# Kernel optimization log

Hardware: AMD Instinct MI355X
Metric: run time of the kernel (lower is better)

The kernel has to match this reference:

```python
import jax, jax.numpy as jnp
import numpy as np

B, S, E = 2, 8192, 128


def setup_inputs() -> dict:
    key = jax.random.key(0)
    ks = jax.random.split(key, 7)
    sc = 1.0 / np.sqrt(E)
    return {
        "x": jax.random.normal(ks[0], (B, S, E), dtype=jnp.float32),
        "Wq": jax.random.normal(ks[1], (E, E), dtype=jnp.float32) * sc,
        "bq": jax.random.normal(ks[2], (E,), dtype=jnp.float32) * 0.01,
        "Wk": jax.random.normal(ks[3], (E, E), dtype=jnp.float32) * sc,
        "bk": jax.random.normal(ks[4], (E,), dtype=jnp.float32) * 0.01,
        "Wv": jax.random.normal(ks[5], (E, E), dtype=jnp.float32) * sc,
        "bv": jax.random.normal(ks[6], (E,), dtype=jnp.float32) * 0.01,
    }


def reference(x, Wq, bq, Wk, bk, Wv, bv):
    # x: [B, S, E]. Conv1d(k=1) == per-slice linear: out[b,s,o] = sum_e W[o,e] x[b,s,e] + b[o]
    embed_dim = x.shape[-1]
    Q = jnp.einsum("bse,oe->bso", x, Wq) + bq  # [B, S, E]
    K = jnp.einsum("bse,oe->bso", x, Wk) + bk
    V = jnp.einsum("bse,oe->bso", x, Wv) + bv
    scores = jnp.einsum("bsd,btd->bst", Q, K) / jnp.sqrt(
        jnp.asarray(embed_dim, dtype=x.dtype)
    )  # [B, S, S]
    A = jax.nn.softmax(scores, axis=-1)
    # torch: out = bmm(V^T_as[B,E,S], A^T)[.transpose] == sum_t A[b,s,t] V[b,t,e]
    out = jnp.einsum("bst,bte->bse", A, V)  # [B, S, E]
    return out
```

## Files before the change

### kernel.cpp

```cpp
#include <hip/hip_runtime.h>
#include <math.h>

#define NB 2
#define NS 8192
#define NE 128
#define NROWS (NB * NS)

typedef __attribute__((ext_vector_type(8))) short s8v;
typedef __attribute__((ext_vector_type(16))) float fx16;
typedef __attribute__((ext_vector_type(2))) unsigned int u2v;
typedef __attribute__((address_space(1))) const unsigned char as1c;
typedef __attribute__((address_space(3))) unsigned char as3t;

static __device__ __forceinline__ unsigned int pkbf(float a, float b) {
    unsigned int ua = __float_as_uint(a), ub = __float_as_uint(b);
    ua += 0x7FFFu + ((ua >> 16) & 1u);
    ub += 0x7FFFu + ((ub >> 16) & 1u);
    return (ua >> 16) | (ub & 0xFFFF0000u);
}

static __device__ __forceinline__ unsigned int cvtpk(float a, float b) {
    unsigned int r;
    asm("v_cvt_pk_bf16_f32 %0, %1, %2" : "=v"(r) : "v"(a), "v"(b));
    return r;
}

static __device__ __forceinline__ void split8(const float* p, uint4& H, uint4& L) {
    float4 a = *(const float4*)p;
    float4 b = *(const float4*)(p + 4);
    unsigned int h0 = cvtpk(a.x, a.y), h1 = cvtpk(a.z, a.w);
    unsigned int h2 = cvtpk(b.x, b.y), h3 = cvtpk(b.z, b.w);
    H = make_uint4(h0, h1, h2, h3);
    float l0 = a.x - __uint_as_float(h0 << 16);
    float l1 = a.y - __uint_as_float(h0 & 0xFFFF0000u);
    float l2 = a.z - __uint_as_float(h1 << 16);
    float l3 = a.w - __uint_as_float(h1 & 0xFFFF0000u);
    float l4 = b.x - __uint_as_float(h2 << 16);
    float l5 = b.y - __uint_as_float(h2 & 0xFFFF0000u);
    float l6 = b.z - __uint_as_float(h3 << 16);
    float l7 = b.w - __uint_as_float(h3 & 0xFFFF0000u);
    L = make_uint4(cvtpk(l0, l1), cvtpk(l2, l3), cvtpk(l4, l5), cvtpk(l6, l7));
}

__global__ __launch_bounds__(256, 4)
void split_kernel(const float* __restrict__ x,
                  const float* __restrict__ Wq, const float* __restrict__ Wk,
                  const float* __restrict__ Wv,
                  unsigned short* __restrict__ xh, unsigned short* __restrict__ xl,
                  unsigned short* __restrict__ WhS, unsigned short* __restrict__ WlS)
{
    const int bid = blockIdx.x;
    if (bid < 1024) {
        const int i = (bid * 256 + threadIdx.x) * 8;
        uint4 H, L;
        split8(&x[i], H, L);
        *(uint4*)&xh[i] = H;
        *(uint4*)&xl[i] = L;
    } else {
        const int tid = (bid - 1024) * 256 + threadIdx.x;
        const int mat = tid >> 11;
        const int rem = tid & 2047;
        const int r = rem >> 4, g = rem & 15;
        const float* W = (mat == 0) ? Wq : (mat == 1) ? Wk : Wv;
        uint4 H, L;
        split8(&W[r * 128 + g * 8], H, L);
        const int gs = g ^ (r & 7);
        *(uint4*)&WhS[mat * 16384 + r * 128 + gs * 8] = H;
        *(uint4*)&WlS[mat * 16384 + r * 128 + gs * 8] = L;
    }
}

__global__ __launch_bounds__(256, 2)
void qkv_kernel(const unsigned short* __restrict__ xh,
                const unsigned short* __restrict__ xl,
                const unsigned short* __restrict__ WhS,
                const unsigned short* __restrict__ WlS,
                const float* __restrict__ bq, const float* __restrict__ bk,
                const float* __restrict__ bv,
                unsigned short* __restrict__ qkv)
{
    __shared__ unsigned short xhL[64 * 128];
    __shared__ unsigned short xlL[64 * 128];
    __shared__ unsigned short WhL[64 * 128];
    __shared__ unsigned short WlL[64 * 128];

    const int t    = threadIdx.x;
    const int rblk = blockIdx.x * 64;
    const int mat  = blockIdx.y;
    const int o0   = blockIdx.z * 64;

    const float* bias = (mat == 0) ? bq : (mat == 1) ? bk : bv;
    unsigned short* out = qkv + (size_t)mat * NROWS * NE;
    const float osc = (mat == 0) ? 0.1275174460620886f : 1.0f;

    const int w = t >> 6, lane = t & 63, lq = lane & 31, h = lane >> 5;

    if (w < 2) {
        const unsigned short* src = (w == 0) ? xh : xl;
        unsigned short* dst = (w == 0) ? xhL : xlL;
        const int rb4 = lane >> 4;
        const int cg  = lane & 15;
        #pragma unroll
        for (int i = 0; i < 16; ++i) {
            const int row = 4 * i + rb4;
            const int c   = cg ^ (row & 7);
            __builtin_amdgcn_global_load_lds(
                (as1c*)(src + (size_t)(rblk + row) * NE + c * 8),
                (as3t*)(dst + i * 512 + lane * 8), 16, 0, 0);
        }
    } else {
        const unsigned short* src = ((w == 2) ? WhS : WlS) + mat * 16384 + o0 * 128;
        unsigned short* dst = (w == 2) ? WhL : WlL;
        #pragma unroll
        for (int i = 0; i < 16; ++i) {
            __builtin_amdgcn_global_load_lds(
                (as1c*)(src + i * 512 + lane * 8),
                (as3t*)(dst + i * 512 + lane * 8), 16, 0, 0);
        }
    }
    __syncthreads();

    const int rloc = (w & 1) * 32;
    const int ot   = w >> 1;

    s8v xhf[8], xlf[8], whf[8], wlf[8];
    #pragma unroll
    for (int s = 0; s < 8; ++s) {
        const int cx = ((s * 2 + h) ^ (lq & 7)) * 8;
        xhf[s] = *(const s8v*)&xhL[(rloc + lq) * 128 + cx];
        xlf[s] = *(const s8v*)&xlL[(rloc + lq) * 128 + cx];
        whf[s] = *(const s8v*)&WhL[(ot * 32 + lq) * 128 + cx];
        wlf[s] = *(const s8v*)&WlL[(ot * 32 + lq) * 128 + cx];
    }

    fx16 acc;
    #pragma unroll
    for (int i = 0; i < 16; ++i) acc[i] = 0.f;

    #pragma unroll
    for (int s = 0; s < 8; ++s) {
        if (mat != 2) {
            acc = __builtin_amdgcn_mfma_f32_32x32x16_bf16(whf[s], xhf[s], acc, 0, 0, 0);
            acc = __builtin_amdgcn_mfma_f32_32x32x16_bf16(whf[s], xlf[s], acc, 0, 0, 0);
            acc = __builtin_amdgcn_mfma_f32_32x32x16_bf16(wlf[s], xhf[s], acc, 0, 0, 0);
        } else {
            acc = __builtin_amdgcn_mfma_f32_32x32x16_bf16(xhf[s], whf[s], acc, 0, 0, 0);
            acc = __builtin_amdgcn_mfma_f32_32x32x16_bf16(xlf[s], whf[s], acc, 0, 0, 0);
            acc = __builtin_amdgcn_mfma_f32_32x32x16_bf16(xhf[s], wlf[s], acc, 0, 0, 0);
        }
    }

    __syncthreads();
    unsigned short* TB = xhL;

    if (mat != 2) {
        #pragma unroll
        for (int g = 0; g < 4; ++g) {
            const int ob = o0 + ot * 32 + 4 * h + 8 * g;
            float4 bb = *(const float4*)&bias[ob];
            float v0 = (acc[4 * g + 0] + bb.x) * osc;
            float v1 = (acc[4 * g + 1] + bb.y) * osc;
            float v2 = (acc[4 * g + 2] + bb.z) * osc;
            float v3 = (acc[4 * g + 3] + bb.w) * osc;
            *(uint2*)&TB[(rloc + lq) * 72 + ot * 32 + 4 * h + 8 * g] =
                make_uint2(pkbf(v0, v1), pkbf(v2, v3));
        }
        __syncthreads();
        #pragma unroll
        for (int it = 0; it < 2; ++it) {
            const int r2 = it * 32 + (t >> 3);
            const int c2 = (t & 7) * 8;
            uint4 vv = *(const uint4*)&TB[r2 * 72 + c2];
            *(uint4*)&out[(size_t)(rblk + r2) * NE + o0 + c2] = vv;
        }
    } else {
        const float bv_ = bias[o0 + ot * 32 + lq];
        #pragma unroll
        for (int g = 0; g < 4; ++g) {
            float v0 = acc[4 * g + 0] + bv_;
            float v1 = acc[4 * g + 1] + bv_;
            float v2 = acc[4 * g + 2] + bv_;
            float v3 = acc[4 * g + 3] + bv_;
            *(uint2*)&TB[(ot * 32 + lq) * 72 + rloc + 4 * h + 8 * g] =
                make_uint2(pkbf(v0, v1), pkbf(v2, v3));
        }
        __syncthreads();
        const int bb_ = rblk >> 13;
        #pragma unroll
        for (int it = 0; it < 2; ++it) {
            const int d2 = it * 32 + (t >> 3);
            const int kc = (t & 7) * 8;
            uint4 vv = *(const uint4*)&TB[d2 * 72 + kc];
            *(uint4*)&out[(((size_t)(bb_ * NE + o0 + d2)) << 13)
                          + (rblk & (NS - 1)) + kc] = vv;
        }
    }
}

__global__ __launch_bounds__(256, 2)
void attn_kernel(const unsigned short* __restrict__ qkv,
                 _Float16* __restrict__ pd,
                 _Float16* __restrict__ pw,
                 float* __restrict__ ml)
{
    __shared__ unsigned short kbuf[2][64 * 128];
    __shared__ unsigned short vbuf[2][64 * 128];

    const int t  = threadIdx.x;
    const int id = blockIdx.x;
    const int ks = id & 3;
    const int b  = (id >> 2) & 1;
    const int T  = id >> 3;

    const unsigned short* Qg = qkv;
    const unsigned short* Kg = qkv + (size_t)NROWS * NE;
    const unsigned short* Vb = qkv + (size_t)2 * NROWS * NE + ((size_t)b << 20);

    const int w = t >> 6, lane = t & 63, lq = lane & 31, h = lane >> 5;
    const int qbw = b * NS + T * 128 + w * 32;
    const size_t kvb = (size_t)b * NS * NE;
    const int kq0 = ks * 2048;

    s8v qf[8];
    #pragma unroll
    for (int s = 0; s < 8; ++s)
        qf[s] = *(const s8v*)(Qg + (size_t)(qbw + lq) * NE + s * 16 + h * 8);

    fx16 acc[4];
    #pragma unroll
    for (int dt = 0; dt < 4; ++dt)
        #pragma unroll
        for (int i = 0; i < 16; ++i) acc[dt][i] = 0.f;

    float l = 0.f;

    const unsigned short* gptr[8];
    if (w < 2) {
        #pragma unroll
        for (int j = 0; j < 8; ++j) {
            int i = 8 * w + j;
            int keyl = 4 * i + (lane >> 4);
            int c = (lane & 15) ^ (keyl & 7);
            gptr[j] = Kg + kvb + (size_t)(kq0 + keyl) * NE + c * 8;
        }
    } else {
        #pragma unroll
        for (int j = 0; j < 8; ++j) {
            int i = 8 * (w - 2) + j;
            int d = 8 * i + (lane >> 3);
            int g = (lane & 7) ^ (d & 7);
            gptr[j] = Vb + ((size_t)d << 13) + kq0 + g * 8;
        }
    }
    const int gstride = (w < 2) ? 64 * NE : 64;

    auto stage = [&](int bufi) {
        if (w < 2) {
            #pragma unroll
            for (int j = 0; j < 8; ++j) {
                __builtin_amdgcn_global_load_lds((as1c*)gptr[j],
                    (as3t*)&kbuf[bufi][(8 * w + j) * 512], 16, 0, 0);
                gptr[j] += gstride;
            }
        } else {
            #pragma unroll
            for (int j = 0; j < 8; ++j) {
                __builtin_amdgcn_global_load_lds((as1c*)gptr[j],
                    (as3t*)&vbuf[bufi][(8 * (w - 2) + j) * 512], 16, 0, 0);
                gptr[j] += gstride;
            }
        }
    };

    stage(0);
    __syncthreads();

#define PEX(i) (st2[(i) >> 4][(i) & 15])
    int buf = 0;
    const int swz = (lq & 7) * 8;

    for (int r = 0; r < 32; ++r) {
        if (r < 31) stage(buf ^ 1);

        fx16 st2[2];
        #pragma unroll
        for (int mt = 0; mt < 2; ++mt)
            #pragma unroll
            for (int i = 0; i < 16; ++i) st2[mt][i] = 0.f;
        __builtin_amdgcn_s_setprio(1);
        #pragma unroll
        for (int s = 0; s < 8; ++s) {
            int co = ((s * 2 + h) * 8) ^ swz;
            s8v a0 = *(const s8v*)&kbuf[buf][lq * 128 + co];
            s8v a1 = *(const s8v*)&kbuf[buf][(32 + lq) * 128 + co];
            st2[0] = __builtin_amdgcn_mfma_f32_32x32x16_bf16(a0, qf[s], st2[0], 0, 0, 0);
            st2[1] = __builtin_amdgcn_mfma_f32_32x32x16_bf16(a1, qf[s], st2[1], 0, 0, 0);
        }
        __builtin_amdgcn_s_setprio(0);

        float a0s = 0.f, a1s = 0.f, a2s = 0.f, a3s = 0.f;
        #pragma unroll
        for (int i = 0; i < 32; i += 4) {
            PEX(i)     = __builtin_amdgcn_exp2f(PEX(i));
            PEX(i + 1) = __builtin_amdgcn_exp2f(PEX(i + 1));
            PEX(i + 2) = __builtin_amdgcn_exp2f(PEX(i + 2));
            PEX(i + 3) = __builtin_amdgcn_exp2f(PEX(i + 3));
            a0s += PEX(i); a1s += PEX(i + 1); a2s += PEX(i + 2); a3s += PEX(i + 3);
        }
        float lsum = (a0s + a1s) + (a2s + a3s);
        lsum += __shfl_xor(lsum, 32);
        l += lsum;

        #pragma unroll
        for (int s2 = 0; s2 < 4; ++s2) {
            unsigned int P0 = cvtpk(PEX(s2 * 8 + 0), PEX(s2 * 8 + 1));
            unsigned int P1 = cvtpk(PEX(s2 * 8 + 2), PEX(s2 * 8 + 3));
            unsigned int P2 = cvtpk(PEX(s2 * 8 + 4), PEX(s2 * 8 + 5));
            unsigned int P3 = cvtpk(PEX(s2 * 8 + 6), PEX(s2 * 8 + 7));
            u2v r02 = __builtin_amdgcn_permlane32_swap(P0, P2, false, false);
            u2v r13 = __builtin_amdgcn_permlane32_swap(P1, P3, false, false);
            union { unsigned int u[4]; s8v v; } pf;
            pf.u[0] = r02.x;
            pf.u[1] = r13.x;
            pf.u[2] = r02.y;
            pf.u[3] = r13.y;
            int go = ((s2 * 2 + h) * 8) ^ swz;
            __builtin_amdgcn_s_setprio(1);
            #pragma unroll
            for (int dt = 0; dt < 4; ++dt) {
                s8v vf = *(const s8v*)&vbuf[buf][(lq + 32 * dt) * 64 + go];
                acc[dt] = __builtin_amdgcn_mfma_f32_32x32x16_bf16(pf.v, vf, acc[dt], 0, 0, 0);
            }
            __builtin_amdgcn_s_setprio(0);
        }

        __syncthreads();
        buf ^= 1;
    }
#undef PEX

    if (lane < 32)
        ml[(size_t)(qbw + lq) * 4 + ks] = l;

    float invl = 1.0f / l;
    _Float16* P = (ks < 2) ? pd : pw;
    const int slot = (ks & 1) * 128;
    #pragma unroll
    for (int rg = 0; rg < 16; ++rg) {
        int row = (rg & 3) + 8 * (rg >> 2) + 4 * h;
        float sc = __shfl(invl, row);
        size_t rb = (size_t)(qbw + row) * 256 + slot;
        #pragma unroll
        for (int dt = 0; dt < 4; ++dt)
            P[rb + lq + 32 * dt] = (_Float16)(acc[dt][rg] * sc);
    }
}

__global__ __launch_bounds__(256, 2)
void merge_kernel(const _Float16* __restrict__ pw,
                  const float* __restrict__ ml,
                  float* __restrict__ outp)
{
    const int gi = blockIdx.x * 256 + threadIdx.x;
    const int q = gi >> 4, d0 = (gi & 15) * 8;
    const _Float16* pd = (const _Float16*)outp;

    uint4 u0 = *(const uint4*)&pd[(size_t)q * 256 + d0];
    uint4 u1 = *(const uint4*)&pd[(size_t)q * 256 + 128 + d0];
    uint4 u2 = *(const uint4*)&pw[(size_t)q * 256 + d0];
    uint4 u3 = *(const uint4*)&pw[(size_t)q * 256 + 128 + d0];
    float l0 = ml[q * 4 + 0], l1 = ml[q * 4 + 1];
    float l2 = ml[q * 4 + 2], l3 = ml[q * 4 + 3];

    float inv = 1.f / (l0 + l1 + l2 + l3);
    float a0 = l0 * inv, a1 = l1 * inv, a2 = l2 * inv, a3 = l3 * inv;

    union { uint4 u; _Float16 hh[8]; } c0, c1, c2, c3;
    c0.u = u0; c1.u = u1; c2.u = u2; c3.u = u3;
    float ov[8];
    #pragma unroll
    for (int e = 0; e < 8; ++e)
        ov[e] = (float)c0.hh[e] * a0 + (float)c1.hh[e] * a1 +
                (float)c2.hh[e] * a2 + (float)c3.hh[e] * a3;

    *(float4*)&outp[(size_t)q * 128 + d0]     = *(float4*)&ov[0];
    *(float4*)&outp[(size_t)q * 128 + d0 + 4] = *(float4*)&ov[4];
}

extern "C" void kernel_launch(void* const* d_in, const int* in_sizes, int n_in,
                              void* d_out, int out_size, void* d_ws, size_t ws_size,
                              hipStream_t stream)
{
    const float* x  = (const float*)d_in[0];
    const float* Wq = (const float*)d_in[1];
    const float* bq = (const float*)d_in[2];
    const float* Wk = (const float*)d_in[3];
    const float* bk = (const float*)d_in[4];
    const float* Wv = (const float*)d_in[5];
    const float* bv = (const float*)d_in[6];
    float* out = (float*)d_out;

    unsigned char* ws = (unsigned char*)d_ws;
    unsigned short* qkv = (unsigned short*)ws;
    _Float16* pw = (_Float16*)(ws + (size_t)3 * NROWS * NE * 2);
    float* mlp = (float*)(ws + (size_t)3 * NROWS * NE * 2
                             + (size_t)NROWS * 256 * 2);
    unsigned char* ws2 = ws + (size_t)3 * NROWS * NE * 2
                            + (size_t)NROWS * 256 * 2 + (size_t)NROWS * 16;
    unsigned short* xh  = (unsigned short*)ws2;
    unsigned short* xl  = xh + (size_t)NROWS * NE;
    unsigned short* WhS = xl + (size_t)NROWS * NE;
    unsigned short* WlS = WhS + 3 * NE * NE;

    split_kernel<<<1048, 256, 0, stream>>>(x, Wq, Wk, Wv, xh, xl, WhS, WlS);

    dim3 g1(NROWS / 64, 3, 2);
    qkv_kernel<<<g1, 256, 0, stream>>>(xh, xl, WhS, WlS, bq, bk, bv, qkv);

    attn_kernel<<<512, 256, 0, stream>>>(qkv, (_Float16*)d_out, pw, mlp);
    merge_kernel<<<1024, 256, 0, stream>>>(pw, mlp, out);
}
```

Baseline: 164.1 us.

## Software-pipeline attention loop so next QK^T overlaps softmax and PV

Splits the per-tile loop into separate QK^T, softmax and PV stages and unrolls it by two with two score register sets. The QK^T MFMAs for the next key tile are issued while the current tile's exp and PV work proceeds. K and V staging are decoupled so K can be prefetched one tile ahead of V. The aim is to hide exp/transcendental latency and LDS waits behind matrix-core work, at the cost of extra registers, which may reduce occupancy.

```diff
diff --git a/kernel.cpp b/kernel.cpp
--- a/kernel.cpp
+++ b/kernel.cpp
@@ -254,7 +254,7 @@
     }
     const int gstride = (w < 2) ? 64 * NE : 64;
 
-    auto stage = [&](int bufi) {
+    auto stageK = [&](int bufi) {
         if (w < 2) {
             #pragma unroll
             for (int j = 0; j < 8; ++j) {
@@ -262,7 +262,10 @@
                     (as3t*)&kbuf[bufi][(8 * w + j) * 512], 16, 0, 0);
                 gptr[j] += gstride;
             }
-        } else {
+        }
+    };
+    auto stageV = [&](int bufi) {
+        if (w >= 2) {
             #pragma unroll
             for (int j = 0; j < 8; ++j) {
                 __builtin_amdgcn_global_load_lds((as1c*)gptr[j],
@@ -272,51 +275,49 @@
         }
     };
 
-    stage(0);
-    __syncthreads();
-
-#define PEX(i) (st2[(i) >> 4][(i) & 15])
-    int buf = 0;
     const int swz = (lq & 7) * 8;
 
-    for (int r = 0; r < 32; ++r) {
-        if (r < 31) stage(buf ^ 1);
-
-        fx16 st2[2];
+    auto gemm1 = [&](fx16 (&st)[2], int bufi) {
         #pragma unroll
         for (int mt = 0; mt < 2; ++mt)
             #pragma unroll
-            for (int i = 0; i < 16; ++i) st2[mt][i] = 0.f;
+            for (int i = 0; i < 16; ++i) st[mt][i] = 0.f;
         __builtin_amdgcn_s_setprio(1);
         #pragma unroll
         for (int s = 0; s < 8; ++s) {
             int co = ((s * 2 + h) * 8) ^ swz;
-            s8v a0 = *(const s8v*)&kbuf[buf][lq * 128 + co];
-            s8v a1 = *(const s8v*)&kbuf[buf][(32 + lq) * 128 + co];
-            st2[0] = __builtin_amdgcn_mfma_f32_32x32x16_bf16(a0, qf[s], st2[0], 0, 0, 0);
-            st2[1] = __builtin_amdgcn_mfma_f32_32x32x16_bf16(a1, qf[s], st2[1], 0, 0, 0);
+            s8v a0 = *(const s8v*)&kbuf[bufi][lq * 128 + co];
+            s8v a1 = *(const s8v*)&kbuf[bufi][(32 + lq) * 128 + co];
+            st[0] = __builtin_amdgcn_mfma_f32_32x32x16_bf16(a0, qf[s], st[0], 0, 0, 0);
+            st[1] = __builtin_amdgcn_mfma_f32_32x32x16_bf16(a1, qf[s], st[1], 0, 0, 0);
         }
         __builtin_amdgcn_s_setprio(0);
-
+    };
+
+#define PEX(st, i) (st[(i) >> 4][(i) & 15])
+    auto smax = [&](fx16 (&st)[2]) {
         float a0s = 0.f, a1s = 0.f, a2s = 0.f, a3s = 0.f;
         #pragma unroll
         for (int i = 0; i < 32; i += 4) {
-            PEX(i)     = __builtin_amdgcn_exp2f(PEX(i));
-            PEX(i + 1) = __builtin_amdgcn_exp2f(PEX(i + 1));
-            PEX(i + 2) = __builtin_amdgcn_exp2f(PEX(i + 2));
-            PEX(i + 3) = __builtin_amdgcn_exp2f(PEX(i + 3));
-            a0s += PEX(i); a1s += PEX(i + 1); a2s += PEX(i + 2); a3s += PEX(i + 3);
+            PEX(st, i)     = __builtin_amdgcn_exp2f(PEX(st, i));
+            PEX(st, i + 1) = __builtin_amdgcn_exp2f(PEX(st, i + 1));
+            PEX(st, i + 2) = __builtin_amdgcn_exp2f(PEX(st, i + 2));
+            PEX(st, i + 3) = __builtin_amdgcn_exp2f(PEX(st, i + 3));
+            a0s += PEX(st, i); a1s += PEX(st, i + 1);
+            a2s += PEX(st, i + 2); a3s += PEX(st, i + 3);
         }
         float lsum = (a0s + a1s) + (a2s + a3s);
         lsum += __shfl_xor(lsum, 32);
         l += lsum;
-
+    };
+
+    auto gemm2 = [&](fx16 (&st)[2], int bufi) {
         #pragma unroll
         for (int s2 = 0; s2 < 4; ++s2) {
-            unsigned int P0 = cvtpk(PEX(s2 * 8 + 0), PEX(s2 * 8 + 1));
-            unsigned int P1 = cvtpk(PEX(s2 * 8 + 2), PEX(s2 * 8 + 3));
-            unsigned int P2 = cvtpk(PEX(s2 * 8 + 4), PEX(s2 * 8 + 5));
-            unsigned int P3 = cvtpk(PEX(s2 * 8 + 6), PEX(s2 * 8 + 7));
+            unsigned int P0 = cvtpk(PEX(st, s2 * 8 + 0), PEX(st, s2 * 8 + 1));
+            unsigned int P1 = cvtpk(PEX(st, s2 * 8 + 2), PEX(st, s2 * 8 + 3));
+            unsigned int P2 = cvtpk(PEX(st, s2 * 8 + 4), PEX(st, s2 * 8 + 5));
+            unsigned int P3 = cvtpk(PEX(st, s2 * 8 + 6), PEX(st, s2 * 8 + 7));
             u2v r02 = __builtin_amdgcn_permlane32_swap(P0, P2, false, false);
             u2v r13 = __builtin_amdgcn_permlane32_swap(P1, P3, false, false);
             union { unsigned int u[4]; s8v v; } pf;
@@ -328,14 +329,37 @@
             __builtin_amdgcn_s_setprio(1);
             #pragma unroll
             for (int dt = 0; dt < 4; ++dt) {
-                s8v vf = *(const s8v*)&vbuf[buf][(lq + 32 * dt) * 64 + go];
+                s8v vf = *(const s8v*)&vbuf[bufi][(lq + 32 * dt) * 64 + go];
                 acc[dt] = __builtin_amdgcn_mfma_f32_32x32x16_bf16(pf.v, vf, acc[dt], 0, 0, 0);
             }
             __builtin_amdgcn_s_setprio(0);
         }
-
+    };
+
+    stageK(0);
+    stageV(0);
+    __syncthreads();
+    fx16 stA[2], stB[2];
+    gemm1(stA, 0);
+    stageK(1);
+    __syncthreads();
+
+    for (int r2 = 0; r2 < 16; ++r2) {
+        const bool notlast = (r2 < 15);
+        if (notlast) stageK(0);
+        stageV(1);
+        smax(stA);
+        gemm1(stB, 1);
+        gemm2(stA, 0);
         __syncthreads();
-        buf ^= 1;
+        if (notlast) {
+            stageK(1);
+            stageV(0);
+        }
+        smax(stB);
+        if (notlast) gemm1(stA, 0);
+        gemm2(stB, 1);
+        __syncthreads();
     }
 #undef PEX
 
```

Result: no change. 163.8 us (-0.1%).

## Split attention keys eight ways and single-buffer V to raise occupancy

Applied to the files above, without the earlier changes.

The split-K factor of the attention kernel goes from 4 to 8, doubling the grid to 1024 blocks. The V LDS buffer is now single-buffered, which cuts shared memory so three blocks can fit per CU. V is loaded at the start of each iteration, with an extra barrier before the PV MFMAs. The merge kernel now combines eight partial outputs through a larger fp16 workspace, so more partials are written and read. Exposed V load latency and the extra sync per iteration could offset the occupancy gain.

```diff
diff --git a/kernel.cpp b/kernel.cpp
--- a/kernel.cpp
+++ b/kernel.cpp
@@ -197,20 +197,20 @@
     }
 }
 
-__global__ __launch_bounds__(256, 2)
+__global__ __launch_bounds__(256, 3)
 void attn_kernel(const unsigned short* __restrict__ qkv,
                  _Float16* __restrict__ pd,
                  _Float16* __restrict__ pw,
                  float* __restrict__ ml)
 {
     __shared__ unsigned short kbuf[2][64 * 128];
-    __shared__ unsigned short vbuf[2][64 * 128];
+    __shared__ unsigned short vbuf[64 * 128];
 
     const int t  = threadIdx.x;
     const int id = blockIdx.x;
-    const int ks = id & 3;
-    const int b  = (id >> 2) & 1;
-    const int T  = id >> 3;
+    const int ks = id & 7;
+    const int b  = (id >> 3) & 1;
+    const int T  = id >> 4;
 
     const unsigned short* Qg = qkv;
     const unsigned short* Kg = qkv + (size_t)NROWS * NE;
@@ -219,7 +219,7 @@
     const int w = t >> 6, lane = t & 63, lq = lane & 31, h = lane >> 5;
     const int qbw = b * NS + T * 128 + w * 32;
     const size_t kvb = (size_t)b * NS * NE;
-    const int kq0 = ks * 2048;
+    const int kq0 = ks * 1024;
 
     s8v qf[8];
     #pragma unroll
@@ -254,7 +254,7 @@
     }
     const int gstride = (w < 2) ? 64 * NE : 64;
 
-    auto stage = [&](int bufi) {
+    auto stageK = [&](int bufi) {
         if (w < 2) {
             #pragma unroll
             for (int j = 0; j < 8; ++j) {
@@ -262,25 +262,30 @@
                     (as3t*)&kbuf[bufi][(8 * w + j) * 512], 16, 0, 0);
                 gptr[j] += gstride;
             }
-        } else {
+        }
+    };
+    auto stageV = [&]() {
+        if (w >= 2) {
             #pragma unroll
             for (int j = 0; j < 8; ++j) {
                 __builtin_amdgcn_global_load_lds((as1c*)gptr[j],
-                    (as3t*)&vbuf[bufi][(8 * (w - 2) + j) * 512], 16, 0, 0);
+                    (as3t*)&vbuf[(8 * (w - 2) + j) * 512], 16, 0, 0);
                 gptr[j] += gstride;
             }
         }
     };
 
-    stage(0);
+    const int swz = (lq & 7) * 8;
+
+    stageK(0);
     __syncthreads();
 
 #define PEX(i) (st2[(i) >> 4][(i) & 15])
     int buf = 0;
-    const int swz = (lq & 7) * 8;
-
-    for (int r = 0; r < 32; ++r) {
-        if (r < 31) stage(buf ^ 1);
+
+    for (int r = 0; r < 16; ++r) {
+        stageV();
+        if (r < 15) stageK(buf ^ 1);
 
         fx16 st2[2];
         #pragma unroll
@@ -310,6 +315,8 @@
         float lsum = (a0s + a1s) + (a2s + a3s);
         lsum += __shfl_xor(lsum, 32);
         l += lsum;
+
+        __syncthreads();
 
         #pragma unroll
         for (int s2 = 0; s2 < 4; ++s2) {
@@ -328,7 +335,7 @@
             __builtin_amdgcn_s_setprio(1);
             #pragma unroll
             for (int dt = 0; dt < 4; ++dt) {
-                s8v vf = *(const s8v*)&vbuf[buf][(lq + 32 * dt) * 64 + go];
+                s8v vf = *(const s8v*)&vbuf[(lq + 32 * dt) * 64 + go];
                 acc[dt] = __builtin_amdgcn_mfma_f32_32x32x16_bf16(pf.v, vf, acc[dt], 0, 0, 0);
             }
             __builtin_amdgcn_s_setprio(0);
@@ -340,16 +347,18 @@
 #undef PEX
 
     if (lane < 32)
-        ml[(size_t)(qbw + lq) * 4 + ks] = l;
+        ml[(size_t)(qbw + lq) * 8 + ks] = l;
 
     float invl = 1.0f / l;
-    _Float16* P = (ks < 2) ? pd : pw;
-    const int slot = (ks & 1) * 128;
+    _Float16* P;
+    int rstride, slot;
+    if (ks < 2) { P = pd; rstride = 256; slot = ks * 128; }
+    else        { P = pw; rstride = 768; slot = (ks - 2) * 128; }
     #pragma unroll
     for (int rg = 0; rg < 16; ++rg) {
         int row = (rg & 3) + 8 * (rg >> 2) + 4 * h;
         float sc = __shfl(invl, row);
-        size_t rb = (size_t)(qbw + row) * 256 + slot;
+        size_t rb = (size_t)(qbw + row) * rstride + slot;
         #pragma unroll
         for (int dt = 0; dt < 4; ++dt)
             P[rb + lq + 32 * dt] = (_Float16)(acc[dt][rg] * sc);
@@ -365,23 +374,28 @@
     const int q = gi >> 4, d0 = (gi & 15) * 8;
     const _Float16* pd = (const _Float16*)outp;
 
-    uint4 u0 = *(const uint4*)&pd[(size_t)q * 256 + d0];
-    uint4 u1 = *(const uint4*)&pd[(size_t)q * 256 + 128 + d0];
-    uint4 u2 = *(const uint4*)&pw[(size_t)q * 256 + d0];
-    uint4 u3 = *(const uint4*)&pw[(size_t)q * 256 + 128 + d0];
-    float l0 = ml[q * 4 + 0], l1 = ml[q * 4 + 1];
-    float l2 = ml[q * 4 + 2], l3 = ml[q * 4 + 3];
-
-    float inv = 1.f / (l0 + l1 + l2 + l3);
-    float a0 = l0 * inv, a1 = l1 * inv, a2 = l2 * inv, a3 = l3 * inv;
-
-    union { uint4 u; _Float16 hh[8]; } c0, c1, c2, c3;
-    c0.u = u0; c1.u = u1; c2.u = u2; c3.u = u3;
+    union { uint4 u; _Float16 hh[8]; } c[8];
+    c[0].u = *(const uint4*)&pd[(size_t)q * 256 + d0];
+    c[1].u = *(const uint4*)&pd[(size_t)q * 256 + 128 + d0];
+    #pragma unroll
+    for (int p = 0; p < 6; ++p)
+        c[2 + p].u = *(const uint4*)&pw[(size_t)q * 768 + p * 128 + d0];
+
+    float4 la = *(const float4*)&ml[q * 8];
+    float4 lb = *(const float4*)&ml[q * 8 + 4];
+    float inv = 1.f / ((la.x + la.y + la.z + la.w) + (lb.x + lb.y + lb.z + lb.w));
+    float wg[8] = { la.x * inv, la.y * inv, la.z * inv, la.w * inv,
+                    lb.x * inv, lb.y * inv, lb.z * inv, lb.w * inv };
+
     float ov[8];
     #pragma unroll
-    for (int e = 0; e < 8; ++e)
-        ov[e] = (float)c0.hh[e] * a0 + (float)c1.hh[e] * a1 +
-                (float)c2.hh[e] * a2 + (float)c3.hh[e] * a3;
+    for (int e = 0; e < 8; ++e) {
+        float s = 0.f;
+        #pragma unroll
+        for (int p = 0; p < 8; ++p)
+            s += (float)c[p].hh[e] * wg[p];
+        ov[e] = s;
+    }
 
     *(float4*)&outp[(size_t)q * 128 + d0]     = *(float4*)&ov[0];
     *(float4*)&outp[(size_t)q * 128 + d0 + 4] = *(float4*)&ov[4];
@@ -404,9 +418,9 @@
     unsigned short* qkv = (unsigned short*)ws;
     _Float16* pw = (_Float16*)(ws + (size_t)3 * NROWS * NE * 2);
     float* mlp = (float*)(ws + (size_t)3 * NROWS * NE * 2
-                             + (size_t)NROWS * 256 * 2);
+                             + (size_t)NROWS * 768 * 2);
     unsigned char* ws2 = ws + (size_t)3 * NROWS * NE * 2
-                            + (size_t)NROWS * 256 * 2 + (size_t)NROWS * 16;
+                            + (size_t)NROWS * 768 * 2 + (size_t)NROWS * 32;
     unsigned short* xh  = (unsigned short*)ws2;
     unsigned short* xl  = xh + (size_t)NROWS * NE;
     unsigned short* WhS = xl + (size_t)NROWS * NE;
@@ -417,6 +431,6 @@
     dim3 g1(NROWS / 64, 3, 2);
     qkv_kernel<<<g1, 256, 0, stream>>>(xh, xl, WhS, WlS, bq, bk, bv, qkv);
 
-    attn_kernel<<<512, 256, 0, stream>>>(qkv, (_Float16*)d_out, pw, mlp);
+    attn_kernel<<<1024, 256, 0, stream>>>(qkv, (_Float16*)d_out, pw, mlp);
     merge_kernel<<<1024, 256, 0, stream>>>(pw, mlp, out);
 }
```

After: 171.1 us. 1.04x slower.
